# Optimization experiments

Measured on AMD Instinct MI355X. Metric: run time of the kernel, lower is better.

The kernel has to match this reference:

```python
import jax, jax.numpy as jnp
import numpy as np

B, N, FEAT, HID, H = 4, 2048, 512, 512, 8
HD = HID // H  # head_dim = 64


def rotate_half(x):
    # pairs along last dim: (x1, x2) -> (-x2, x1), interleaved
    x = x.reshape(*x.shape[:-1], -1, 2)
    x1, x2 = x[..., 0], x[..., 1]
    return jnp.stack((-x2, x1), axis=-1).reshape(*x.shape[:-2], -1)


def apply_rope(freqs, t):
    # freqs: [2, B, 1, N, HD] broadcasting over heads; t: [B, H, N, HD]
    return t * freqs[0] + rotate_half(t) * freqs[1]


def setup_inputs() -> dict:
    key = jax.random.key(0)
    ks = jax.random.split(key, 12)
    s = 0.02
    return {
        "x0": jax.random.normal(ks[0], (B, N, FEAT), jnp.float32),
        "x1": jax.random.normal(ks[1], (B, N, FEAT), jnp.float32),
        "encoding0": jax.random.normal(ks[2], (2, B, 1, N, HD), jnp.float32),
        "encoding1": jax.random.normal(ks[3], (2, B, 1, N, HD), jnp.float32),
        "Wqkv": jax.random.normal(ks[4], (FEAT, 3 * HID), jnp.float32) * s,
        "bqkv": jnp.zeros((3 * HID,), jnp.float32),
        "Wproj": jax.random.normal(ks[5], (HID, HID), jnp.float32) * s,
        "bproj": jnp.zeros((HID,), jnp.float32),
        "W1": jax.random.normal(ks[6], (FEAT + HID, 2 * FEAT), jnp.float32) * s,
        "b1": jnp.zeros((2 * FEAT,), jnp.float32),
        "ln_g": jnp.ones((2 * FEAT,), jnp.float32),
        "ln_b": jnp.zeros((2 * FEAT,), jnp.float32),
        "W2": jax.random.normal(ks[7], (2 * FEAT, FEAT), jnp.float32) * s,
        "b2": jnp.zeros((FEAT,), jnp.float32),
    }


def _block(x, enc, Wqkv, bqkv, Wproj, bproj, W1, b1, ln_g, ln_b, W2, b2):
    b, n, _ = x.shape
    qkv = x @ Wqkv + bqkv                                   # [B,N,3*HID]
    qkv = qkv.reshape(b, n, H, HD, 3).transpose(0, 2, 1, 3, 4)  # [B,H,N,HD,3]
    q, k, v = qkv[..., 0], qkv[..., 1], qkv[..., 2]
    q = apply_rope(enc, q)
    k = apply_rope(enc, k)
    scale = q.shape[-1] ** (-0.5)
    attn = jax.nn.softmax(jnp.einsum('bhid,bhjd->bhij', q, k) * scale, axis=-1)
    o = jnp.einsum('bhij,bhjd->bhid', attn, v)              # [B,H,N,HD]
    message = o.transpose(0, 2, 1, 3).reshape(b, n, HID) @ Wproj + bproj
    h = jnp.concatenate([x, message], axis=-1) @ W1 + b1    # [B,N,2*FEAT]
    mu = h.mean(-1, keepdims=True)
    var = ((h - mu) ** 2).mean(-1, keepdims=True)
    h = (h - mu) * jax.lax.rsqrt(var + 1e-5) * ln_g + ln_b
    return x + jax.nn.gelu(h, approximate=False) @ W2 + b2


def reference(x0, x1, encoding0, encoding1, Wqkv, bqkv, Wproj, bproj, W1, b1, ln_g, ln_b, W2, b2):
    p = (Wqkv, bqkv, Wproj, bproj, W1, b1, ln_g, ln_b, W2, b2)
    return (_block(x0, encoding0, *p), _block(x1, encoding1, *p))
```

## Files before the change

kernel.cpp:

```cpp
#include <hip/hip_runtime.h>
#include <hip/hip_bf16.h>

typedef __attribute__((ext_vector_type(8))) short   short8v;
typedef __attribute__((ext_vector_type(8))) __bf16  bf16x8;
typedef __attribute__((ext_vector_type(4))) float   f32x4;

constexpr int Nn = 2048;

#define GLOAD_LDS(src, dst) \
  __builtin_amdgcn_global_load_lds((__attribute__((address_space(1))) unsigned int*)(src), \
                                   (__attribute__((address_space(3))) unsigned int*)(dst), 16, 0, 0)

#if __has_builtin(__builtin_amdgcn_exp2f)
#define EXP2F(x) __builtin_amdgcn_exp2f(x)
#else
#define EXP2F(x) exp2f(x)
#endif

__device__ __forceinline__ unsigned pack_bf16(float lo, float hi) {
  union { __bf16 h[2]; unsigned u; } t;
  t.h[0] = (__bf16)lo; t.h[1] = (__bf16)hi;
  return t.u;
}

template<int AMODE, int EPI>
__global__ __launch_bounds__(256)
void gemm_mfma(const __bf16* __restrict__ A, const __bf16* __restrict__ A2,
               const __bf16* __restrict__ BT,
               const float* __restrict__ bias,
               const float* __restrict__ resid0, const float* __restrict__ resid1,
               float* __restrict__ Cf, __bf16* __restrict__ Cb, __bf16* __restrict__ Vt,
               int lda, int ldb, int ldc, int K1, int K)
{
  __shared__ __align__(16) __bf16 As[128 * 32];
  __shared__ __align__(16) __bf16 Bs[128 * 32];
  const int tid = threadIdx.x;
  const int w = tid >> 6, l = tid & 63;
  const int wr = w >> 1, wc = w & 1;
  const int lr = l & 15, lg = l >> 4;
  const int row0 = blockIdx.x * 128, col0 = blockIdx.y * 128;

  f32x4 acc[4][4];
#pragma unroll
  for (int i = 0; i < 4; ++i)
#pragma unroll
    for (int j = 0; j < 4; ++j) acc[i][j] = (f32x4){0.f, 0.f, 0.f, 0.f};

  const int srow = l >> 2;
  const int skk  = (l & 3) * 8;

  for (int k0 = 0; k0 < K; k0 += 32) {
    for (int s = w; s < 8; s += 4) {
      const int m = s * 16 + srow;
      const __bf16* src;
      if constexpr (AMODE == 0) {
        src = A + (size_t)(row0 + m) * lda + k0 + skk;
      } else {
        const int gk = k0 + skk;
        src = (gk < K1) ? A  + (size_t)(row0 + m) * lda + gk
                        : A2 + (size_t)(row0 + m) * lda + (gk - K1);
      }
      GLOAD_LDS(src, &As[s * 512]);
    }
    for (int s = w; s < 8; s += 4) {
      const int n = s * 16 + srow;
      GLOAD_LDS(BT + (size_t)(col0 + n) * ldb + k0 + skk, &Bs[s * 512]);
    }
    __syncthreads();
    bf16x8 af[4], bfv[4];
#pragma unroll
    for (int mi = 0; mi < 4; ++mi)
      af[mi] = *(const bf16x8*)&As[(wr * 64 + mi * 16 + lr) * 32 + lg * 8];
#pragma unroll
    for (int ni = 0; ni < 4; ++ni)
      bfv[ni] = *(const bf16x8*)&Bs[(wc * 64 + ni * 16 + lr) * 32 + lg * 8];
    __builtin_amdgcn_s_setprio(1);
#pragma unroll
    for (int mi = 0; mi < 4; ++mi)
#pragma unroll
      for (int ni = 0; ni < 4; ++ni)
        acc[mi][ni] = __builtin_amdgcn_mfma_f32_16x16x32_bf16(af[mi], bfv[ni], acc[mi][ni], 0, 0, 0);
    __builtin_amdgcn_s_setprio(0);
    __syncthreads();
  }

  if constexpr (EPI == 4) {
    if (col0 >= 1024) {
      const int b2 = row0 >> 11;
#pragma unroll
      for (int mi = 0; mi < 4; ++mi)
#pragma unroll
        for (int ni = 0; ni < 4; ++ni) {
          const int col = col0 + wc * 64 + ni * 16 + lr;
          const int sec = col - 1024, h = sec >> 6, d = sec & 63;
          const int n0 = (row0 + wr * 64 + mi * 16 + lg * 4) & 2047;
          union { __bf16 h4[4]; short4 s4; } u;
#pragma unroll
          for (int r = 0; r < 4; ++r) u.h4[r] = (__bf16)(acc[mi][ni][r] + bias[col]);
          *(short4*)&Vt[(size_t)(b2 * 8 + h) * 131072 + (size_t)d * 2048 + n0] = u.s4;
        }
    } else {
#pragma unroll
      for (int mi = 0; mi < 4; ++mi)
#pragma unroll
        for (int ni = 0; ni < 4; ++ni) {
          const int col = col0 + wc * 64 + ni * 16 + lr;
#pragma unroll
          for (int r = 0; r < 4; ++r) {
            const int row = row0 + wr * 64 + mi * 16 + lg * 4 + r;
            Cb[(size_t)row * 1024 + col] = (__bf16)(acc[mi][ni][r] + bias[col]);
          }
        }
    }
    return;
  }

#pragma unroll
  for (int mi = 0; mi < 4; ++mi)
#pragma unroll
    for (int ni = 0; ni < 4; ++ni) {
      const int col = col0 + wc * 64 + ni * 16 + lr;
#pragma unroll
      for (int r = 0; r < 4; ++r) {
        const int row = row0 + wr * 64 + mi * 16 + lg * 4 + r;
        const float v = acc[mi][ni][r];
        if constexpr (EPI == 1) {
          Cb[(size_t)row * ldc + col] = (__bf16)(v + bias[col]);
        } else {
          const float* rp = (row < 8192) ? resid0 : resid1;
          Cf[(size_t)row * ldc + col] = v + bias[col] + rp[(size_t)(row & 8191) * ldc + col];
        }
      }
    }
}

__global__ __launch_bounds__(256, 2)
void fa_k(const __bf16* __restrict__ QK, const __bf16* __restrict__ Vg,
          __bf16* __restrict__ Ob)
{
  __shared__ __align__(16) __bf16 Ks[8192];
  __shared__ __align__(16) __bf16 Vs[8192];
  const int tid = threadIdx.x;
  const int w = tid >> 6, l = tid & 63;
  const int lr = l & 15, lg = l >> 4;
  const int bh = blockIdx.y;
  const int b2 = bh >> 3, h = bh & 7;
  const __bf16* Qp = QK + (size_t)b2 * 2048 * 1024 + h * 64;
  const __bf16* Kp = Qp + 512;
  const __bf16* Vp = Vg + (size_t)bh * 131072;
  const int q0 = blockIdx.x * 128 + w * 32;

  bf16x8 qf[2][2];
#pragma unroll
  for (int nf = 0; nf < 2; ++nf)
#pragma unroll
    for (int kk = 0; kk < 2; ++kk)
      qf[nf][kk] = *(const bf16x8*)&Qp[(size_t)(q0 + nf * 16 + lr) * 1024 + kk * 32 + lg * 8];

  f32x4 oacc[4][2];
#pragma unroll
  for (int i = 0; i < 4; ++i)
#pragma unroll
    for (int j = 0; j < 2; ++j) oacc[i][j] = (f32x4){0.f, 0.f, 0.f, 0.f};
  float m_run[2] = {-1e30f, -1e30f}, lsum[2] = {0.f, 0.f};

  const int Sa = (lg & 1) * 32 + lr, Sb2 = Sa + 16;
  const bool hi = (lg >> 1) & 1;
  constexpr float SC = 0.125f * 1.44269504089f;

  for (int kv0 = 0; kv0 < 2048; kv0 += 128) {
#pragma unroll
    for (int i = 0; i < 4; ++i) {
      const int s = w + 4 * i;
      { const int g = s * 64 + l, r = g >> 3, c = g & 7;
        GLOAD_LDS(Kp + (size_t)(kv0 + r) * 1024 + ((c ^ (r & 7)) * 8), &Ks[s * 512]); }
      { const int g = s * 64 + l, r = g >> 4, c = g & 15;
        GLOAD_LDS(Vp + (size_t)r * 2048 + kv0 + ((c ^ (r & 15)) * 8), &Vs[s * 512]); }
    }
    __syncthreads();

    f32x4 sacc[8][2];
#pragma unroll
    for (int i = 0; i < 8; ++i)
#pragma unroll
      for (int j = 0; j < 2; ++j) sacc[i][j] = (f32x4){0.f, 0.f, 0.f, 0.f};
#pragma unroll
    for (int kk = 0; kk < 2; ++kk) {
      bf16x8 ka[8];
#pragma unroll
      for (int mf = 0; mf < 8; ++mf)
        ka[mf] = *(const bf16x8*)&Ks[(mf * 16 + lr) * 64 + (((kk * 4 + lg) ^ (lr & 7)) * 8)];
      __builtin_amdgcn_s_setprio(1);
#pragma unroll
      for (int mf = 0; mf < 8; ++mf)
#pragma unroll
        for (int nf = 0; nf < 2; ++nf)
          sacc[mf][nf] = __builtin_amdgcn_mfma_f32_16x16x32_bf16(ka[mf], qf[nf][kk], sacc[mf][nf], 0, 0, 0);
      __builtin_amdgcn_s_setprio(0);
    }

    unsigned pk[8][2][2];
#pragma unroll
    for (int nf = 0; nf < 2; ++nf) {
      float tm = -1e30f;
#pragma unroll
      for (int mf = 0; mf < 8; ++mf)
#pragma unroll
        for (int r = 0; r < 4; ++r) {
          sacc[mf][nf][r] *= SC;
          tm = fmaxf(tm, sacc[mf][nf][r]);
        }
      tm = fmaxf(tm, __shfl_xor(tm, 16, 64));
      tm = fmaxf(tm, __shfl_xor(tm, 32, 64));
      if (__any(tm > m_run[nf] + 8.f)) {
        const float mn = fmaxf(m_run[nf], tm);
        const float corr = EXP2F(m_run[nf] - mn);
        m_run[nf] = mn;
        lsum[nf] *= corr;
#pragma unroll
        for (int mo = 0; mo < 4; ++mo)
#pragma unroll
          for (int r = 0; r < 4; ++r) oacc[mo][nf][r] *= corr;
      }
      const float mcur = m_run[nf];
      float rs = 0.f;
#pragma unroll
      for (int mf = 0; mf < 8; ++mf) {
        const float p0 = EXP2F(sacc[mf][nf][0] - mcur);
        const float p1 = EXP2F(sacc[mf][nf][1] - mcur);
        const float p2 = EXP2F(sacc[mf][nf][2] - mcur);
        const float p3 = EXP2F(sacc[mf][nf][3] - mcur);
        rs += (p0 + p1) + (p2 + p3);
        pk[mf][nf][0] = pack_bf16(p0, p1);
        pk[mf][nf][1] = pack_bf16(p2, p3);
      }
      rs += __shfl_xor(rs, 16, 64);
      rs += __shfl_xor(rs, 32, 64);
      lsum[nf] += rs;
    }

#pragma unroll
    for (int kf = 0; kf < 4; ++kf) {
      bf16x8 va[4];
#pragma unroll
      for (int mo = 0; mo < 4; ++mo)
        va[mo] = *(const bf16x8*)&Vs[(mo * 16 + lr) * 128 + ((((kf * 4 + lg) ^ lr) & 15) * 8)];
      bf16x8 bfr[2];
#pragma unroll
      for (int nf = 0; nf < 2; ++nf) {
        const unsigned s0 = hi ? pk[kf * 2 + 1][nf][0] : pk[kf * 2][nf][0];
        const unsigned s1 = hi ? pk[kf * 2 + 1][nf][1] : pk[kf * 2][nf][1];
        union { unsigned u[4]; bf16x8 v; } ub;
        ub.u[0] = (unsigned)__shfl((int)s0, Sa, 64);
        ub.u[1] = (unsigned)__shfl((int)s1, Sa, 64);
        ub.u[2] = (unsigned)__shfl((int)s0, Sb2, 64);
        ub.u[3] = (unsigned)__shfl((int)s1, Sb2, 64);
        bfr[nf] = ub.v;
      }
      __builtin_amdgcn_s_setprio(1);
#pragma unroll
      for (int mo = 0; mo < 4; ++mo)
#pragma unroll
        for (int nf = 0; nf < 2; ++nf)
          oacc[mo][nf] = __builtin_amdgcn_mfma_f32_16x16x32_bf16(va[mo], bfr[nf], oacc[mo][nf], 0, 0, 0);
      __builtin_amdgcn_s_setprio(0);
    }
    __syncthreads();
  }

#pragma unroll
  for (int nf = 0; nf < 2; ++nf) {
    const float inv = 1.f / lsum[nf];
    const long row = (long)b2 * 2048 + q0 + nf * 16 + lr;
#pragma unroll
    for (int mo = 0; mo < 4; ++mo) {
      union { __bf16 h4[4]; short4 s4; } u;
#pragma unroll
      for (int r = 0; r < 4; ++r) u.h4[r] = (__bf16)(oacc[mo][nf][r] * inv);
      *(short4*)&Ob[row * 512 + h * 64 + mo * 16 + lg * 4] = u.s4;
    }
  }
}

__global__ __launch_bounds__(256)
void conv_f32_bf16_k(const float* __restrict__ s, __bf16* __restrict__ d)
{
  const long i = ((long)blockIdx.x * 256 + threadIdx.x) * 4;
  const float4 v = *(const float4*)&s[i];
  union { __bf16 h[4]; short4 sv; } u;
  u.h[0] = (__bf16)v.x; u.h[1] = (__bf16)v.y; u.h[2] = (__bf16)v.z; u.h[3] = (__bf16)v.w;
  *(short4*)&d[i] = u.sv;
}

template<int PERM>
__global__ __launch_bounds__(256)
void transpose_wt_k(const float* __restrict__ W, __bf16* __restrict__ WT, int K, int N)
{
  __shared__ float t[32][33];
  const int n0 = blockIdx.x * 32, k0 = blockIdx.y * 32;
  const int tx = threadIdx.x & 31, ty = threadIdx.x >> 5;
  for (int i = ty; i < 32; i += 8)
    t[i][tx] = W[(size_t)(k0 + i) * N + n0 + tx];
  __syncthreads();
  for (int i = ty; i < 32; i += 8) {
    int drow = n0 + i;
    if constexpr (PERM) {
      const int h = drow / 192, rem = drow % 192;
      drow = (rem % 3) * 512 + h * 64 + rem / 3;
    }
    WT[(size_t)drow * K + k0 + tx] = (__bf16)t[tx][i];
  }
}

__global__ void bperm_k(const float* __restrict__ b, float* __restrict__ bp)
{
  const int i = blockIdx.x * 256 + threadIdx.x;
  if (i < 1536) {
    const int h = i / 192, rem = i % 192;
    bp[(rem % 3) * 512 + h * 64 + rem / 3] = b[i];
  }
}

__global__ __launch_bounds__(256)
void rope_k(__bf16* __restrict__ qkvb, const float* __restrict__ enc0,
            const float* __restrict__ enc1)
{
  const long idx = (long)blockIdx.x * 256 + threadIdx.x;
  const int t = (int)(idx & 31);
  const int h = (int)((idx >> 5) & 7);
  const long row = idx >> 8;
  const long bn = row & 8191;
  const float* e = (row < 8192) ? enc0 : enc1;
  const int d0 = 2 * t;
  const float f0a = e[bn * 64 + d0], f0b = e[bn * 64 + d0 + 1];
  const float f1a = e[524288 + bn * 64 + d0], f1b = e[524288 + bn * 64 + d0 + 1];
  const long base = row * 1024 + (long)h * 64 + d0;
#pragma unroll
  for (int s = 0; s < 2; ++s) {
    union { __bf16 hx[2]; unsigned u; } p;
    p.u = *(unsigned*)&qkvb[base + s * 512];
    const float x0 = (float)p.hx[0], x1 = (float)p.hx[1];
    p.hx[0] = (__bf16)(x0 * f0a - x1 * f1a);
    p.hx[1] = (__bf16)(x1 * f0b + x0 * f1b);
    *(unsigned*)&qkvb[base + s * 512] = p.u;
  }
}

__global__ __launch_bounds__(256)
void ln_gelu_k(__bf16* __restrict__ Hb, const float* __restrict__ g,
               const float* __restrict__ be)
{
  __bf16* row = Hb + (size_t)blockIdx.x * 1024;
  const int tid = threadIdx.x;
  __shared__ float rs_[256], rq_[256];
  union { __bf16 h[4]; short4 sv; } u;
  u.sv = *(const short4*)&row[tid * 4];
  float v[4];
  float s = 0.f, sq = 0.f;
#pragma unroll
  for (int i = 0; i < 4; ++i) {
    v[i] = (float)u.h[i];
    s += v[i]; sq += v[i] * v[i];
  }
  rs_[tid] = s; rq_[tid] = sq; __syncthreads();
  for (int st = 128; st > 0; st >>= 1) {
    if (tid < st) { rs_[tid] += rs_[tid + st]; rq_[tid] += rq_[tid + st]; }
    __syncthreads();
  }
  const float mu = rs_[0] * (1.f / 1024.f);
  const float var = rq_[0] * (1.f / 1024.f) - mu * mu;
  const float rstd = rsqrtf(var + 1e-5f);
#pragma unroll
  for (int i = 0; i < 4; ++i) {
    const int c = tid * 4 + i;
    const float y = (v[i] - mu) * rstd * g[c] + be[c];
    u.h[i] = (__bf16)(0.5f * y * (1.f + erff(y * 0.70710678118f)));
  }
  *(short4*)&row[tid * 4] = u.sv;
}

extern "C" void kernel_launch(void* const* d_in, const int* in_sizes, int n_in,
                              void* d_out, int out_size, void* d_ws, size_t ws_size,
                              hipStream_t stream)
{
  const float* x0   = (const float*)d_in[0];
  const float* x1   = (const float*)d_in[1];
  const float* enc0 = (const float*)d_in[2];
  const float* enc1 = (const float*)d_in[3];
  const float* Wqkv  = (const float*)d_in[4];
  const float* bqkv  = (const float*)d_in[5];
  const float* Wproj = (const float*)d_in[6];
  const float* bproj = (const float*)d_in[7];
  const float* W1    = (const float*)d_in[8];
  const float* b1    = (const float*)d_in[9];
  const float* ln_g  = (const float*)d_in[10];
  const float* ln_b  = (const float*)d_in[11];
  const float* W2    = (const float*)d_in[12];
  const float* b2    = (const float*)d_in[13];

  __bf16* wsb = (__bf16*)d_ws;
  __bf16* xb     = wsb;
  __bf16* WqkvT  = wsb + 8388608;
  __bf16* WprojT = wsb + 9175040;
  __bf16* W1T    = wsb + 9437184;
  __bf16* W2T    = wsb + 10485760;
  float*  bqkvp  = (float*)(wsb + 11010048);
  __bf16* qkvb   = wsb + 11013120;
  __bf16* Vt     = wsb + 27790336;
  __bf16* Ob     = wsb + 36178944;
  __bf16* msgb   = qkvb;
  __bf16* hb     = Vt;

  transpose_wt_k<1><<<dim3(48, 16), 256, 0, stream>>>(Wqkv, WqkvT, 512, 1536);
  transpose_wt_k<0><<<dim3(16, 16), 256, 0, stream>>>(Wproj, WprojT, 512, 512);
  transpose_wt_k<0><<<dim3(32, 32), 256, 0, stream>>>(W1, W1T, 1024, 1024);
  transpose_wt_k<0><<<dim3(16, 32), 256, 0, stream>>>(W2, W2T, 1024, 512);
  bperm_k<<<6, 256, 0, stream>>>(bqkv, bqkvp);

  conv_f32_bf16_k<<<4096, 256, 0, stream>>>(x0, xb);
  conv_f32_bf16_k<<<4096, 256, 0, stream>>>(x1, xb + 4194304);

  gemm_mfma<0, 4><<<dim3(128, 12), 256, 0, stream>>>(
      xb, nullptr, WqkvT, bqkvp, nullptr, nullptr, nullptr, qkvb, Vt,
      512, 512, 1024, 0, 512);
  rope_k<<<16384, 256, 0, stream>>>(qkvb, enc0, enc1);
  fa_k<<<dim3(16, 64), 256, 0, stream>>>(qkvb, Vt, Ob);
  gemm_mfma<0, 1><<<dim3(128, 4), 256, 0, stream>>>(
      Ob, nullptr, WprojT, bproj, nullptr, nullptr, nullptr, msgb, nullptr,
      512, 512, 512, 0, 512);
  gemm_mfma<1, 1><<<dim3(128, 8), 256, 0, stream>>>(
      xb, msgb, W1T, b1, nullptr, nullptr, nullptr, hb, nullptr,
      512, 1024, 1024, 512, 1024);
  ln_gelu_k<<<16384, 256, 0, stream>>>(hb, ln_g, ln_b);
  gemm_mfma<0, 2><<<dim3(128, 4), 256, 0, stream>>>(
      hb, nullptr, W2T, b2, x0, x1, (float*)d_out, nullptr, nullptr,
      1024, 1024, 512, 0, 1024);
}
```

Before: 357.4 us.

## Double-buffer flash-attention K/V tiles and use 16x16x16 MFMA for PV

The attention kernel now keeps two LDS buffers for K and V and issues the global-to-LDS loads for the next KV tile before computing on the current one, with explicit vmcnt waits and raw barriers. This is meant to hide load latency behind compute. The PV product switches to the 16x16x16 bf16 MFMA when that builtin exists, so the packed P registers can be fed directly without cross-lane shuffles. The softmax scale is folded into Q inside the rope kernel, which removes a per-element multiply in the attention loop. The cost is double the LDS per block, which may lower occupancy, plus a small precision change from rounding the pre-scaled Q to bf16.

```diff
diff --git a/kernel.cpp b/kernel.cpp
--- a/kernel.cpp
+++ b/kernel.cpp
@@ -2,7 +2,9 @@
 #include <hip/hip_bf16.h>
 
 typedef __attribute__((ext_vector_type(8))) short   short8v;
+typedef __attribute__((ext_vector_type(4))) short   short4v;
 typedef __attribute__((ext_vector_type(8))) __bf16  bf16x8;
+typedef __attribute__((ext_vector_type(4))) __bf16  bf16x4;
 typedef __attribute__((ext_vector_type(4))) float   f32x4;
 
 constexpr int Nn = 2048;
@@ -15,6 +17,13 @@
 #define EXP2F(x) __builtin_amdgcn_exp2f(x)
 #else
 #define EXP2F(x) exp2f(x)
+#endif
+
+#if __has_builtin(__builtin_amdgcn_mfma_f32_16x16x16bf16_1k)
+#define HAVE_MFMA16 1
+#define MFMA16(a, b, c) __builtin_amdgcn_mfma_f32_16x16x16bf16_1k(a, b, c, 0, 0, 0)
+#else
+#define HAVE_MFMA16 0
 #endif
 
 __device__ __forceinline__ unsigned pack_bf16(float lo, float hi) {
@@ -138,8 +147,8 @@
 void fa_k(const __bf16* __restrict__ QK, const __bf16* __restrict__ Vg,
           __bf16* __restrict__ Ob)
 {
-  __shared__ __align__(16) __bf16 Ks[8192];
-  __shared__ __align__(16) __bf16 Vs[8192];
+  __shared__ __align__(16) __bf16 Ks[2][8192];
+  __shared__ __align__(16) __bf16 Vs[2][8192];
   const int tid = threadIdx.x;
   const int w = tid >> 6, l = tid & 63;
   const int lr = l & 15, lg = l >> 4;
@@ -164,20 +173,35 @@
     for (int j = 0; j < 2; ++j) oacc[i][j] = (f32x4){0.f, 0.f, 0.f, 0.f};
   float m_run[2] = {-1e30f, -1e30f}, lsum[2] = {0.f, 0.f};
 
-  const int Sa = (lg & 1) * 32 + lr, Sb2 = Sa + 16;
+#if !HAVE_MFMA16
+  const int Sa = (lg & 1) * 32 + lr, Sb2x = Sa + 16;
   const bool hi = (lg >> 1) & 1;
-  constexpr float SC = 0.125f * 1.44269504089f;
-
-  for (int kv0 = 0; kv0 < 2048; kv0 += 128) {
+#endif
+
+  auto stage = [&](int kv0, int b) {
 #pragma unroll
     for (int i = 0; i < 4; ++i) {
       const int s = w + 4 * i;
       { const int g = s * 64 + l, r = g >> 3, c = g & 7;
-        GLOAD_LDS(Kp + (size_t)(kv0 + r) * 1024 + ((c ^ (r & 7)) * 8), &Ks[s * 512]); }
+        GLOAD_LDS(Kp + (size_t)(kv0 + r) * 1024 + ((c ^ (r & 7)) * 8), &Ks[b][s * 512]); }
       { const int g = s * 64 + l, r = g >> 4, c = g & 15;
-        GLOAD_LDS(Vp + (size_t)r * 2048 + kv0 + ((c ^ (r & 15)) * 8), &Vs[s * 512]); }
-    }
-    __syncthreads();
+        GLOAD_LDS(Vp + (size_t)r * 2048 + kv0 + ((c ^ (r & 15)) * 8), &Vs[b][s * 512]); }
+    }
+  };
+
+  stage(0, 0);
+
+  for (int t = 0; t < 16; ++t) {
+    const int p = t & 1;
+    if (t < 15) {
+      stage((t + 1) * 128, 1 - p);
+      asm volatile("s_waitcnt vmcnt(8)" ::: "memory");
+    } else {
+      asm volatile("s_waitcnt vmcnt(0)" ::: "memory");
+    }
+    __builtin_amdgcn_sched_barrier(0);
+    __builtin_amdgcn_s_barrier();
+    __builtin_amdgcn_sched_barrier(0);
 
     f32x4 sacc[8][2];
 #pragma unroll
@@ -189,7 +213,7 @@
       bf16x8 ka[8];
 #pragma unroll
       for (int mf = 0; mf < 8; ++mf)
-        ka[mf] = *(const bf16x8*)&Ks[(mf * 16 + lr) * 64 + (((kk * 4 + lg) ^ (lr & 7)) * 8)];
+        ka[mf] = *(const bf16x8*)&Ks[p][(mf * 16 + lr) * 64 + (((kk * 4 + lg) ^ (lr & 7)) * 8)];
       __builtin_amdgcn_s_setprio(1);
 #pragma unroll
       for (int mf = 0; mf < 8; ++mf)
@@ -199,17 +223,14 @@
       __builtin_amdgcn_s_setprio(0);
     }
 
-    unsigned pk[8][2][2];
+    unsigned pkk[8][2][2];
 #pragma unroll
     for (int nf = 0; nf < 2; ++nf) {
       float tm = -1e30f;
 #pragma unroll
       for (int mf = 0; mf < 8; ++mf)
 #pragma unroll
-        for (int r = 0; r < 4; ++r) {
-          sacc[mf][nf][r] *= SC;
-          tm = fmaxf(tm, sacc[mf][nf][r]);
-        }
+        for (int r = 0; r < 4; ++r) tm = fmaxf(tm, sacc[mf][nf][r]);
       tm = fmaxf(tm, __shfl_xor(tm, 16, 64));
       tm = fmaxf(tm, __shfl_xor(tm, 32, 64));
       if (__any(tm > m_run[nf] + 8.f)) {
@@ -231,30 +252,50 @@
         const float p2 = EXP2F(sacc[mf][nf][2] - mcur);
         const float p3 = EXP2F(sacc[mf][nf][3] - mcur);
         rs += (p0 + p1) + (p2 + p3);
-        pk[mf][nf][0] = pack_bf16(p0, p1);
-        pk[mf][nf][1] = pack_bf16(p2, p3);
+        pkk[mf][nf][0] = pack_bf16(p0, p1);
+        pkk[mf][nf][1] = pack_bf16(p2, p3);
       }
       rs += __shfl_xor(rs, 16, 64);
       rs += __shfl_xor(rs, 32, 64);
       lsum[nf] += rs;
     }
 
+#if HAVE_MFMA16
+#pragma unroll
+    for (int ks = 0; ks < 8; ++ks) {
+      bf16x4 va[4];
+#pragma unroll
+      for (int mo = 0; mo < 4; ++mo) {
+        const int og = 2 * ks + (lg >> 1);
+        va[mo] = *(const bf16x4*)&Vs[p][(mo * 16 + lr) * 128 + ((og ^ lr) & 15) * 8 + (lg & 1) * 4];
+      }
+      __builtin_amdgcn_s_setprio(1);
+#pragma unroll
+      for (int mo = 0; mo < 4; ++mo)
+#pragma unroll
+        for (int nf = 0; nf < 2; ++nf)
+          oacc[mo][nf] = MFMA16(__builtin_bit_cast(short4v, va[mo]),
+                                __builtin_bit_cast(short4v, pkk[ks][nf]),
+                                oacc[mo][nf]);
+      __builtin_amdgcn_s_setprio(0);
+    }
+#else
 #pragma unroll
     for (int kf = 0; kf < 4; ++kf) {
       bf16x8 va[4];
 #pragma unroll
       for (int mo = 0; mo < 4; ++mo)
-        va[mo] = *(const bf16x8*)&Vs[(mo * 16 + lr) * 128 + ((((kf * 4 + lg) ^ lr) & 15) * 8)];
+        va[mo] = *(const bf16x8*)&Vs[p][(mo * 16 + lr) * 128 + ((((kf * 4 + lg) ^ lr) & 15) * 8)];
       bf16x8 bfr[2];
 #pragma unroll
       for (int nf = 0; nf < 2; ++nf) {
-        const unsigned s0 = hi ? pk[kf * 2 + 1][nf][0] : pk[kf * 2][nf][0];
-        const unsigned s1 = hi ? pk[kf * 2 + 1][nf][1] : pk[kf * 2][nf][1];
+        const unsigned s0 = hi ? pkk[kf * 2 + 1][nf][0] : pkk[kf * 2][nf][0];
+        const unsigned s1 = hi ? pkk[kf * 2 + 1][nf][1] : pkk[kf * 2][nf][1];
         union { unsigned u[4]; bf16x8 v; } ub;
         ub.u[0] = (unsigned)__shfl((int)s0, Sa, 64);
         ub.u[1] = (unsigned)__shfl((int)s1, Sa, 64);
-        ub.u[2] = (unsigned)__shfl((int)s0, Sb2, 64);
-        ub.u[3] = (unsigned)__shfl((int)s1, Sb2, 64);
+        ub.u[2] = (unsigned)__shfl((int)s0, Sb2x, 64);
+        ub.u[3] = (unsigned)__shfl((int)s1, Sb2x, 64);
         bfr[nf] = ub.v;
       }
       __builtin_amdgcn_s_setprio(1);
@@ -265,7 +306,8 @@
           oacc[mo][nf] = __builtin_amdgcn_mfma_f32_16x16x32_bf16(va[mo], bfr[nf], oacc[mo][nf], 0, 0, 0);
       __builtin_amdgcn_s_setprio(0);
     }
-    __syncthreads();
+#endif
+    __builtin_amdgcn_s_barrier();
   }
 
 #pragma unroll
@@ -325,6 +367,7 @@
 void rope_k(__bf16* __restrict__ qkvb, const float* __restrict__ enc0,
             const float* __restrict__ enc1)
 {
+  constexpr float SCQ = 0.125f * 1.44269504089f;
   const long idx = (long)blockIdx.x * 256 + threadIdx.x;
   const int t = (int)(idx & 31);
   const int h = (int)((idx >> 5) & 7);
@@ -335,14 +378,21 @@
   const float f0a = e[bn * 64 + d0], f0b = e[bn * 64 + d0 + 1];
   const float f1a = e[524288 + bn * 64 + d0], f1b = e[524288 + bn * 64 + d0 + 1];
   const long base = row * 1024 + (long)h * 64 + d0;
-#pragma unroll
-  for (int s = 0; s < 2; ++s) {
+  {
     union { __bf16 hx[2]; unsigned u; } p;
-    p.u = *(unsigned*)&qkvb[base + s * 512];
+    p.u = *(unsigned*)&qkvb[base];
+    const float x0 = (float)p.hx[0], x1 = (float)p.hx[1];
+    p.hx[0] = (__bf16)((x0 * f0a - x1 * f1a) * SCQ);
+    p.hx[1] = (__bf16)((x1 * f0b + x0 * f1b) * SCQ);
+    *(unsigned*)&qkvb[base] = p.u;
+  }
+  {
+    union { __bf16 hx[2]; unsigned u; } p;
+    p.u = *(unsigned*)&qkvb[base + 512];
     const float x0 = (float)p.hx[0], x1 = (float)p.hx[1];
     p.hx[0] = (__bf16)(x0 * f0a - x1 * f1a);
     p.hx[1] = (__bf16)(x1 * f0b + x0 * f1b);
-    *(unsigned*)&qkvb[base + s * 512] = p.u;
+    *(unsigned*)&qkvb[base + 512] = p.u;
   }
 }
 
```

Result: no change. 353.6 us (-1.1%).
